# Performance work log

Measured on AMD Instinct MI355X. Metric: run time of the kernel, lower is better.

## Reference

```python
import jax, jax.numpy as jnp
import numpy as np

N_FEATURES = 64
HIDDEN = 512
BATCH = 128
SEQ = 1024


def _lstm_cell(x, h, c, w_ih, w_hh, b_ih, b_hh):
    # PyTorch gate order: input, forget, cell(g), output
    gates = x @ w_ih.T + b_ih + h @ w_hh.T + b_hh  # [B, 4H]
    i, f, g, o = jnp.split(gates, 4, axis=-1)
    c_new = jax.nn.sigmoid(f) * c + jax.nn.sigmoid(i) * jnp.tanh(g)
    h_new = jax.nn.sigmoid(o) * jnp.tanh(c_new)
    return h_new, c_new


def setup_inputs() -> dict:
    key = jax.random.key(0)
    ks = jax.random.split(key, 12)
    s_in = 1.0 / np.sqrt(HIDDEN)
    ts_batch = jax.random.normal(ks[0], (BATCH, SEQ, N_FEATURES), dtype=jnp.float32)
    u = lambda k, shape: jax.random.uniform(k, shape, jnp.float32, -s_in, s_in)
    return {
        "ts_batch": ts_batch,
        "w_ih_enc": u(ks[1], (4 * HIDDEN, N_FEATURES)),
        "w_hh_enc": u(ks[2], (4 * HIDDEN, HIDDEN)),
        "b_ih_enc": u(ks[3], (4 * HIDDEN,)),
        "b_hh_enc": u(ks[4], (4 * HIDDEN,)),
        "w_ih_dec": u(ks[5], (4 * HIDDEN, N_FEATURES)),
        "w_hh_dec": u(ks[6], (4 * HIDDEN, HIDDEN)),
        "b_ih_dec": u(ks[7], (4 * HIDDEN,)),
        "b_hh_dec": u(ks[8], (4 * HIDDEN,)),
        "w_out": u(ks[9], (N_FEATURES, HIDDEN)),
        "b_out": u(ks[10], (N_FEATURES,)),
    }


def reference(ts_batch, w_ih_enc, w_hh_enc, b_ih_enc, b_hh_enc,
              w_ih_dec, w_hh_dec, b_ih_dec, b_hh_dec, w_out, b_out):
    B, T, F = ts_batch.shape
    H = w_hh_enc.shape[1]
    h0 = jnp.zeros((B, H), ts_batch.dtype)
    c0 = jnp.zeros((B, H), ts_batch.dtype)

    # ---- encoder: run LSTM over time, keep final hidden state ----
    def enc_step(carry, x_t):
        h, c = carry
        h, c = _lstm_cell(x_t, h, c, w_ih_enc, w_hh_enc, b_ih_enc, b_hh_enc)
        return (h, c), None

    xs = jnp.transpose(ts_batch, (1, 0, 2))  # [T, B, F]
    (h_enc, _), _ = jax.lax.scan(enc_step, (h0, c0), xs)

    # ---- decoder (eval mode): reversed time, feed own output back ----
    def dec_step(carry, _):
        h, c = carry
        y = h @ w_out.T + b_out  # [B, F], emitted BEFORE the cell update
        h, c = _lstm_cell(y, h, c, w_ih_dec, w_hh_dec, b_ih_dec, b_hh_dec)
        return (h, c), y

    (_, _), ys = jax.lax.scan(dec_step, (h_enc, c0), None, length=T)
    # ys[k] corresponds to output time index T-1-k -> flip to chronological order
    output = jnp.transpose(ys[::-1], (1, 0, 2))  # [B, T, F]
    return output
```

## Files before the change

### kernel.cpp

```cpp
#include <hip/hip_runtime.h>
#include <math.h>

#define BB 128
#define TT 1024
#define FF 64
#define HH 512
#define G4 2048
#define NI 8
#define NJ 32
#define BT 16
#define NBLK 256
#define LDK 520
#define SENT 0xFFFFFFFFu

typedef float f32x4 __attribute__((ext_vector_type(4)));
typedef short s16x8 __attribute__((ext_vector_type(8)));
typedef unsigned short u16;
typedef unsigned int u32;
typedef unsigned long long u64;

__device__ u16 g_tsh[BB * TT * FF];
__device__ u16 g_tsl[BB * TT * FF];
__device__ float g_wihe[G4 * FF];
__device__ float g_whhe[G4 * HH];
__device__ float g_bihe[G4], g_bhhe[G4], g_bihd[G4], g_bhhd[G4];
__device__ float g_wihd[G4 * FF];
__device__ float g_whhd[G4 * HH];
__device__ float g_wout[FF * HH];
__device__ float g_bout[FF];
__device__ float g_weff[G4 * HH];
__device__ float g_beff[G4];
__device__ __align__(16) u64 g_hpak[2 * BB * HH];
__device__ __align__(16) float g_part[4 * NI * NJ * BT * FF];
__device__ int   g_isbf16;

__device__ __forceinline__ float bf2f(u16 u) {
  union { unsigned u; float f; } x; x.u = ((unsigned)u) << 16; return x.f;
}
__device__ __forceinline__ u16 f2bf(float f) {
  union { float f; unsigned u; } x; x.f = f;
  unsigned r = x.u + 0x7fffu + ((x.u >> 16) & 1u);
  return (u16)(r >> 16);
}
__device__ __forceinline__ float fsig(float x) {
  return __builtin_amdgcn_rcpf(1.f + __expf(-x));
}
__device__ __forceinline__ float ftanh(float x) {
  return 1.f - 2.f * __builtin_amdgcn_rcpf(__expf(2.f * x) + 1.f);
}

__global__ void sniff_kernel(const void* wout) {
  __shared__ int cnt[64];
  int t = threadIdx.x;
  const unsigned* d = (const unsigned*)wout;
  int c = 0;
  for (int k = t; k < 1024; k += 64) {
    unsigned b = (d[k] >> 8) & 0x7fu;
    c += (b >= 0x30u && b <= 0x3eu) ? 1 : 0;
  }
  cnt[t] = c;
  __syncthreads();
  if (t == 0) {
    int s = 0;
    for (int k = 0; k < 64; ++k) s += cnt[k];
    g_isbf16 = (s > 512) ? 1 : 0;
  }
}

__global__ void convert_kernel(const void* __restrict__ src, int which, int n) {
  int idx = blockIdx.x * 256 + threadIdx.x;
  if (idx >= n) return;
  float v;
  if (g_isbf16) v = bf2f(((const u16*)src)[idx]);
  else          v = ((const float*)src)[idx];
  if (which == 0) {
    u16 hi = f2bf(v);
    g_tsh[idx] = hi;
    g_tsl[idx] = f2bf(v - bf2f(hi));
    return;
  }
  float* dst;
  switch (which) {
    case 1: dst = g_wihe; break;
    case 2: dst = g_whhe; break;
    case 3: dst = g_bihe; break;
    case 4: dst = g_bhhe; break;
    case 5: dst = g_wihd; break;
    case 6: dst = g_whhd; break;
    case 7: dst = g_bihd; break;
    case 8: dst = g_bhhd; break;
    case 9: dst = g_wout; break;
    default: dst = g_bout; break;
  }
  dst[idx] = v;
}

__global__ void prep_kernel() {
  int idx = blockIdx.x * 256 + threadIdx.x;
  int r = idx >> 9, c = idx & 511;
  float acc = g_whhd[idx];
  const float* wr = &g_wihd[r * FF];
  for (int f = 0; f < FF; ++f) acc += wr[f] * g_wout[f * HH + c];
  g_weff[idx] = acc;
  if (idx < G4) {
    float b = g_bihd[idx] + g_bhhd[idx];
    for (int f = 0; f < FF; ++f) b += g_wihd[idx * FF + f] * g_bout[f];
    g_beff[idx] = b;
  }
}

__global__ void hinit_kernel() {
  int idx = blockIdx.x * 256 + threadIdx.x;
  g_hpak[idx] = (idx < (BB * HH / 2)) ? 0ull : 0xFFFFFFFFFFFFFFFFull;
}

#define MFMA __builtin_amdgcn_mfma_f32_16x16x32_bf16
#define A_LD(p)  __hip_atomic_load((p), __ATOMIC_RELAXED, __HIP_MEMORY_SCOPE_AGENT)
#define A_ST(p, v) __hip_atomic_store((p), (v), __ATOMIC_RELAXED, __HIP_MEMORY_SCOPE_AGENT)

#define BAR() do { asm volatile("s_waitcnt lgkmcnt(0)" ::: "memory"); \
                   __builtin_amdgcn_s_barrier(); } while (0)

#define LDR(R) do { \
    q[4*(R)+0] = A_LD(ph + (R)*256 +   0); \
    q[4*(R)+1] = A_LD(ph + (R)*256 +  64); \
    q[4*(R)+2] = A_LD(ph + (R)*256 + 128); \
    q[4*(R)+3] = A_LD(ph + (R)*256 + 192); } while (0)
#define BADR(R) ( ((u32)q[4*(R)+0]==SENT) | ((u32)(q[4*(R)+0]>>32)==SENT) | \
                  ((u32)q[4*(R)+1]==SENT) | ((u32)(q[4*(R)+1]>>32)==SENT) | \
                  ((u32)q[4*(R)+2]==SENT) | ((u32)(q[4*(R)+2]>>32)==SENT) | \
                  ((u32)q[4*(R)+3]==SENT) | ((u32)(q[4*(R)+3]>>32)==SENT) )

__global__ __launch_bounds__(256, 1) void lstm_persist(void* __restrict__ outv) {
  __shared__ u16 sHB[2][32 * LDK];
  __shared__ float sHn[16][17];
  __shared__ float sWoT[16][64];

  const int tid = threadIdx.x, bid = blockIdx.x;
  const int i = bid & 7, j = bid >> 3;
  const int wv = tid >> 6, lane = tid & 63;
  const int ln15 = lane & 15, lq = lane >> 4;
  const int gc = ln15 >> 2, uc = ln15 & 3;
  const int gr0 = gc * 512 + (j << 4) + (wv << 2) + uc;
  const int tb = gc;
  const int b_own = 4 * lq + tb;
  const int u_own = (wv << 2) + uc;
  const size_t colrow = (size_t)(i * BT + b_own) * (HH / 2) + (j << 3) + (u_own >> 1);
  const bool isbf = (g_isbf16 != 0);

  s16x8 wh[16], wl[16];
#pragma unroll
  for (int kt = 0; kt < 16; ++kt) {
    const float* p = &g_whhe[(size_t)gr0 * HH + kt * 32 + lq * 8];
#pragma unroll
    for (int q = 0; q < 8; ++q) {
      float w = p[q]; u16 hi = f2bf(w);
      wh[kt][q] = (short)hi; wl[kt][q] = (short)f2bf(w - bf2f(hi));
    }
  }
  s16x8 bxh0, bxh1, bxl0, bxl1;
  {
    const float* p0 = &g_wihe[(size_t)gr0 * FF + lq * 8];
#pragma unroll
    for (int q = 0; q < 8; ++q) {
      float w0 = p0[q], w1 = p0[32 + q];
      u16 h0 = f2bf(w0), h1 = f2bf(w1);
      bxh0[q] = (short)h0; bxl0[q] = (short)f2bf(w0 - bf2f(h0));
      bxh1[q] = (short)h1; bxl1[q] = (short)f2bf(w1 - bf2f(h1));
    }
  }
  for (int idx = tid; idx < 16 * 64; idx += 256) {
    int n = idx >> 6, f = idx & 63;
    sWoT[n][f] = g_wout[f * HH + (j << 4) + n];
  }
  float bias = g_bihe[gr0] + g_bhhe[gr0];

  const int e_jj = tid & 31;
  const int e_cell = (j << 3) + (tid >> 5);
  const int e_mm = e_cell >> 4, e_ff = (e_cell & 15) << 2;
  const float eb0 = g_bout[e_ff + 0], eb1 = g_bout[e_ff + 1];
  const float eb2 = g_bout[e_ff + 2], eb3 = g_bout[e_ff + 3];

  float c_st = 0.f;
  const int arow = ln15 * LDK;
  const int koff = lq * 8;

  for (int g = 0; g <= 2048; ++g) {
    const bool run = (g < 2048);
    float hn = 0.f;
    u64 e0 = 0, e1 = 0;
    const bool demit = (g >= 1025);

    if (!run && demit) {
      const int slot = (g - 2) & 3;
      const u64* psrc = (const u64*)&g_part[
          (size_t)((((slot * NI) + i) * NJ + e_jj) * BT + e_mm) * FF + e_ff];
      e0 = A_LD(psrc + 0); e1 = A_LD(psrc + 1);
    }

    if (run) {
      const bool enc = (g < 1024);
      s16x8 xh0 = {}, xl0 = {}, xh1 = {}, xl1 = {};
      if (enc) {
        const size_t xo = ((size_t)(i * BT + ln15) * TT + g) * FF + lq * 8;
        xh0 = *(const s16x8*)&g_tsh[xo];
        xh1 = *(const s16x8*)&g_tsh[xo + 32];
        xl0 = *(const s16x8*)&g_tsl[xo];
        xl1 = *(const s16x8*)&g_tsl[xo + 32];
      }

      u64 q[16];
      {
        const u64* ph = g_hpak
            + (size_t)((g & 3) * BB + i * BT + (wv << 2)) * (HH / 2) + lane;
        LDR(0); LDR(1); LDR(2); LDR(3);
        bool b0 = BADR(0), b1 = BADR(1), b2 = BADR(2), b3 = BADR(3);
        while (b0 | b1 | b2 | b3) {
          __builtin_amdgcn_s_sleep(1);
          if (b0) { LDR(0); b0 = BADR(0); }
          if (b1) { LDR(1); b1 = BADR(1); }
          if (b2) { LDR(2); b2 = BADR(2); }
          if (b3) { LDR(3); b3 = BADR(3); }
        }
      }
      {
        u16* sHw = &sHB[g & 1][0];
#pragma unroll
        for (int r = 0; r < 4; ++r) {
          const int row = (wv << 2) + r;
#pragma unroll
          for (int j2 = 0; j2 < 4; ++j2) {
            u64 v = q[4 * r + j2];
            u32 w0 = (u32)v, w1 = (u32)(v >> 32);
            u32 hi = __builtin_amdgcn_perm(w1, w0, 0x05040100u);
            u32 lo = __builtin_amdgcn_perm(w1, w0, 0x07060302u);
            const int u0 = 128 * j2 + 2 * lane;
            *(u32*)&sHw[row * LDK + u0] = hi;
            *(u32*)&sHw[(16 + row) * LDK + u0] = lo;
          }
        }
      }
      BAR();

      f32x4 a0a = {bias, bias, bias, bias};
      f32x4 a0b = {0.f,0.f,0.f,0.f}, a1a = {0.f,0.f,0.f,0.f}, a1b = {0.f,0.f,0.f,0.f};
      f32x4 a2a = {0.f,0.f,0.f,0.f}, a2b = {0.f,0.f,0.f,0.f};
      const u16* sHb = &sHB[g & 1][0];
#pragma unroll
      for (int kt = 0; kt < 16; kt += 2) {
        {
          s16x8 ah = *(const s16x8*)&sHb[arow + kt * 32 + koff];
          s16x8 al = *(const s16x8*)&sHb[16 * LDK + arow + kt * 32 + koff];
          a0a = MFMA(ah, wh[kt], a0a, 0, 0, 0);
          a1a = MFMA(al, wh[kt], a1a, 0, 0, 0);
          a2a = MFMA(ah, wl[kt], a2a, 0, 0, 0);
        }
        {
          s16x8 ah = *(const s16x8*)&sHb[arow + (kt + 1) * 32 + koff];
          s16x8 al = *(const s16x8*)&sHb[16 * LDK + arow + (kt + 1) * 32 + koff];
          a0b = MFMA(ah, wh[kt + 1], a0b, 0, 0, 0);
          a1b = MFMA(al, wh[kt + 1], a1b, 0, 0, 0);
          a2b = MFMA(ah, wl[kt + 1], a2b, 0, 0, 0);
        }
      }
      if (enc) {
        a0a = MFMA(xh0, bxh0, a0a, 0, 0, 0);
        a0b = MFMA(xh1, bxh1, a0b, 0, 0, 0);
        a1a = MFMA(xl0, bxh0, a1a, 0, 0, 0);
        a1b = MFMA(xl1, bxh1, a1b, 0, 0, 0);
        a2a = MFMA(xh0, bxl0, a2a, 0, 0, 0);
        a2b = MFMA(xh1, bxl1, a2b, 0, 0, 0);
      }
      f32x4 vs = (a0a + a0b) + (a1a + a1b) + (a2a + a2b);

      float A0 = vs.x, A1 = vs.y, A2 = vs.z, A3 = vs.w;
      float t0 = __shfl_xor(A2, 8), t1 = __shfl_xor(A3, 8);
      float t2 = __shfl_xor(A0, 8), t3 = __shfl_xor(A1, 8);
      const bool hi2 = (tb & 2) != 0;
      float B0 = hi2 ? t0 : A0, B1 = hi2 ? t1 : A1;
      float B2 = hi2 ? A2 : t2, B3 = hi2 ? A3 : t3;
      float u0 = __shfl_xor(B1, 4), u1 = __shfl_xor(B0, 4);
      float u2 = __shfl_xor(B3, 4), u3 = __shfl_xor(B2, 4);
      const bool hi1 = (tb & 1) != 0;
      float gi = hi1 ? u0 : B0, gf = hi1 ? B1 : u1;
      float gg = hi1 ? u2 : B2, go = hi1 ? B3 : u3;

      float si = fsig(gi), sf = fsig(gf), tg = ftanh(gg), so_ = fsig(go);
      c_st = sf * c_st + si * tg;
      hn = so_ * ftanh(c_st);
      {
        u16 h0p = f2bf(hn), l0p = f2bf(hn - bf2f(h0p));
        u32 pak = (u32)h0p | ((u32)l0p << 16);
        u32 oth = __shfl_down(pak, 1);
        asm volatile("s_waitcnt vmcnt(0)" ::: "memory");
        if ((ln15 & 1) == 0) {
          A_ST(&g_hpak[(size_t)(((g + 1) & 3)) * (BB * HH / 2) + colrow],
               (u64)pak | ((u64)oth << 32));
          A_ST(&g_hpak[(size_t)(((g + 3) & 3)) * (BB * HH / 2) + colrow],
               0xFFFFFFFFFFFFFFFFull);
        }
      }
      if (demit) {
        const int slot = (g - 2) & 3;
        const u64* psrc = (const u64*)&g_part[
            (size_t)((((slot * NI) + i) * NJ + e_jj) * BT + e_mm) * FF + e_ff];
        e0 = A_LD(psrc + 0); e1 = A_LD(psrc + 1);
      }
    }

    if (g >= 1023 && g < 2047) {
      sHn[b_own][u_own] = hn;
      BAR();
      const int fg = tid & 15, mm = tid >> 4;
      float p0 = 0.f, p1 = 0.f, p2 = 0.f, p3 = 0.f;
#pragma unroll
      for (int n = 0; n < 16; ++n) {
        float hv = sHn[mm][n];
        const f32x4 w = *(const f32x4*)&sWoT[n][fg << 2];
        p0 += hv * w.x; p1 += hv * w.y; p2 += hv * w.z; p3 += hv * w.w;
      }
      union { float f[4]; u64 d[2]; } pu;
      pu.f[0] = p0; pu.f[1] = p1; pu.f[2] = p2; pu.f[3] = p3;
      u64* pp = (u64*)&g_part[(size_t)((((g & 3) * NI + i) * NJ + j) * BT + mm) * FF + (fg << 2)];
      A_ST(pp + 0, pu.d[0]); A_ST(pp + 1, pu.d[1]);
    }
    if (demit) {
      const int k = g - 1025;
      union { u64 d[2]; float f[4]; } uu; uu.d[0] = e0; uu.d[1] = e1;
      float s0 = uu.f[0], s1 = uu.f[1], s2 = uu.f[2], s3 = uu.f[3];
#pragma unroll
      for (int m = 16; m >= 1; m >>= 1) {
        s0 += __shfl_xor(s0, m); s1 += __shfl_xor(s1, m);
        s2 += __shfl_xor(s2, m); s3 += __shfl_xor(s3, m);
      }
      if (e_jj == 0) {
        float o0 = s0 + eb0, o1 = s1 + eb1, o2 = s2 + eb2, o3 = s3 + eb3;
        size_t oidx = ((size_t)(i * BT + e_mm) * TT + (1023 - k)) * FF + e_ff;
        if (isbf) {
          union { u16 h[4]; u64 d; } ov;
          ov.h[0] = f2bf(o0); ov.h[1] = f2bf(o1); ov.h[2] = f2bf(o2); ov.h[3] = f2bf(o3);
          *(u64*)((u16*)outv + oidx) = ov.d;
        } else {
          f32x4 ov = {o0, o1, o2, o3};
          *(f32x4*)((float*)outv + oidx) = ov;
        }
      }
    }

    if (g == 1023) {
#pragma unroll
      for (int kt = 0; kt < 16; ++kt) {
        const float* p = &g_weff[(size_t)gr0 * HH + kt * 32 + lq * 8];
#pragma unroll
        for (int q2 = 0; q2 < 8; ++q2) {
          float w = p[q2]; u16 hi = f2bf(w);
          wh[kt][q2] = (short)hi; wl[kt][q2] = (short)f2bf(w - bf2f(hi));
        }
      }
      bias = g_beff[gr0];
      c_st = 0.f;
    }
  }
}

extern "C" void kernel_launch(void* const* d_in, const int* in_sizes, int n_in,
                              void* d_out, int out_size, void* d_ws, size_t ws_size,
                              hipStream_t stream) {
  sniff_kernel<<<1, 64, 0, stream>>>(d_in[9]);

  const int sizes[11] = { BB * TT * FF, G4 * FF, G4 * HH, G4, G4,
                          G4 * FF, G4 * HH, G4, G4, FF * HH, FF };
  for (int k = 0; k < 11; ++k)
    convert_kernel<<<(sizes[k] + 255) / 256, 256, 0, stream>>>(d_in[k], k, sizes[k]);

  prep_kernel<<<(G4 * HH) / 256, 256, 0, stream>>>();
  hinit_kernel<<<(2 * BB * HH) / 256, 256, 0, stream>>>();

  lstm_persist<<<NBLK, 256, 0, stream>>>(d_out);
}
```

Baseline: 6.235 ms.

## Halve persistent grid to 128 blocks of 512 threads, each owning 32 hidden units

The persistent LSTM kernel now runs 128 blocks of 8 waves instead of 256 blocks of 4 waves, so each block handles 32 hidden units per batch tile instead of 16. Each wave loads and spins on two rows of the shared hidden-state buffer instead of four. The output-projection partials are split into two half-blocks, which keeps the 32-way reduction layout unchanged. The aim is to halve the number of blocks polling global hidden-state flags and to cut redundant h reloads, at the cost of more register and LDS pressure per CU and half as many CUs in use.

```diff
diff --git a/kernel.cpp b/kernel.cpp
--- a/kernel.cpp
+++ b/kernel.cpp
@@ -8,8 +8,10 @@
 #define G4 2048
 #define NI 8
 #define NJ 32
+#define JB 16
 #define BT 16
-#define NBLK 256
+#define NBLK 128
+#define NTHR 512
 #define LDK 520
 #define SENT 0xFFFFFFFFu
 
@@ -32,7 +34,7 @@
 __device__ float g_beff[G4];
 __device__ __align__(16) u64 g_hpak[2 * BB * HH];
 __device__ __align__(16) float g_part[4 * NI * NJ * BT * FF];
-__device__ int   g_isbf16;
+__device__ int g_isbf16;
 
 __device__ __forceinline__ float bf2f(u16 u) {
   union { unsigned u; float f; } x; x.u = ((unsigned)u) << 16; return x.f;
@@ -131,21 +133,21 @@
                   ((u32)q[4*(R)+2]==SENT) | ((u32)(q[4*(R)+2]>>32)==SENT) | \
                   ((u32)q[4*(R)+3]==SENT) | ((u32)(q[4*(R)+3]>>32)==SENT) )
 
-__global__ __launch_bounds__(256, 1) void lstm_persist(void* __restrict__ outv) {
+__global__ __launch_bounds__(NTHR, 1) void lstm_persist(void* __restrict__ outv) {
   __shared__ u16 sHB[2][32 * LDK];
-  __shared__ float sHn[16][17];
-  __shared__ float sWoT[16][64];
+  __shared__ float sHn[16][33];
+  __shared__ float sWoT[32][64];
 
   const int tid = threadIdx.x, bid = blockIdx.x;
   const int i = bid & 7, j = bid >> 3;
   const int wv = tid >> 6, lane = tid & 63;
   const int ln15 = lane & 15, lq = lane >> 4;
   const int gc = ln15 >> 2, uc = ln15 & 3;
-  const int gr0 = gc * 512 + (j << 4) + (wv << 2) + uc;
+  const int gr0 = gc * 512 + (j << 5) + (wv << 2) + uc;
   const int tb = gc;
   const int b_own = 4 * lq + tb;
   const int u_own = (wv << 2) + uc;
-  const size_t colrow = (size_t)(i * BT + b_own) * (HH / 2) + (j << 3) + (u_own >> 1);
+  const size_t colrow = (size_t)(i * BT + b_own) * (HH / 2) + (j << 4) + (u_own >> 1);
   const bool isbf = (g_isbf16 != 0);
 
   s16x8 wh[16], wl[16];
@@ -153,33 +155,36 @@
   for (int kt = 0; kt < 16; ++kt) {
     const float* p = &g_whhe[(size_t)gr0 * HH + kt * 32 + lq * 8];
 #pragma unroll
-    for (int q = 0; q < 8; ++q) {
-      float w = p[q]; u16 hi = f2bf(w);
-      wh[kt][q] = (short)hi; wl[kt][q] = (short)f2bf(w - bf2f(hi));
+    for (int q2 = 0; q2 < 8; ++q2) {
+      float w = p[q2]; u16 hi = f2bf(w);
+      wh[kt][q2] = (short)hi; wl[kt][q2] = (short)f2bf(w - bf2f(hi));
     }
   }
   s16x8 bxh0, bxh1, bxl0, bxl1;
   {
     const float* p0 = &g_wihe[(size_t)gr0 * FF + lq * 8];
 #pragma unroll
-    for (int q = 0; q < 8; ++q) {
-      float w0 = p0[q], w1 = p0[32 + q];
+    for (int q2 = 0; q2 < 8; ++q2) {
+      float w0 = p0[q2], w1 = p0[32 + q2];
       u16 h0 = f2bf(w0), h1 = f2bf(w1);
-      bxh0[q] = (short)h0; bxl0[q] = (short)f2bf(w0 - bf2f(h0));
-      bxh1[q] = (short)h1; bxl1[q] = (short)f2bf(w1 - bf2f(h1));
-    }
-  }
-  for (int idx = tid; idx < 16 * 64; idx += 256) {
+      bxh0[q2] = (short)h0; bxl0[q2] = (short)f2bf(w0 - bf2f(h0));
+      bxh1[q2] = (short)h1; bxl1[q2] = (short)f2bf(w1 - bf2f(h1));
+    }
+  }
+  for (int idx = tid; idx < 32 * 64; idx += NTHR) {
     int n = idx >> 6, f = idx & 63;
-    sWoT[n][f] = g_wout[f * HH + (j << 4) + n];
+    sWoT[n][f] = g_wout[f * HH + (j << 5) + n];
   }
   float bias = g_bihe[gr0] + g_bhhe[gr0];
 
   const int e_jj = tid & 31;
-  const int e_cell = (j << 3) + (tid >> 5);
+  const int e_cell = (j << 4) + (tid >> 5);
   const int e_mm = e_cell >> 4, e_ff = (e_cell & 15) << 2;
   const float eb0 = g_bout[e_ff + 0], eb1 = g_bout[e_ff + 1];
   const float eb2 = g_bout[e_ff + 2], eb3 = g_bout[e_ff + 3];
+
+  const int p_fg = tid & 15, p_half = (tid >> 4) & 1, p_mm = tid >> 5;
+  const int p_n0 = p_half << 4;
 
   float c_st = 0.f;
   const int arow = ln15 * LDK;
@@ -209,32 +214,30 @@
         xl1 = *(const s16x8*)&g_tsl[xo + 32];
       }
 
-      u64 q[16];
+      u64 q[8];
       {
         const u64* ph = g_hpak
-            + (size_t)((g & 3) * BB + i * BT + (wv << 2)) * (HH / 2) + lane;
-        LDR(0); LDR(1); LDR(2); LDR(3);
-        bool b0 = BADR(0), b1 = BADR(1), b2 = BADR(2), b3 = BADR(3);
-        while (b0 | b1 | b2 | b3) {
+            + (size_t)((g & 3) * BB + i * BT + (wv << 1)) * (HH / 2) + lane;
+        LDR(0); LDR(1);
+        bool b0 = BADR(0), b1 = BADR(1);
+        while (b0 | b1) {
           __builtin_amdgcn_s_sleep(1);
           if (b0) { LDR(0); b0 = BADR(0); }
           if (b1) { LDR(1); b1 = BADR(1); }
-          if (b2) { LDR(2); b2 = BADR(2); }
-          if (b3) { LDR(3); b3 = BADR(3); }
         }
       }
       {
         u16* sHw = &sHB[g & 1][0];
 #pragma unroll
-        for (int r = 0; r < 4; ++r) {
-          const int row = (wv << 2) + r;
-#pragma unroll
-          for (int j2 = 0; j2 < 4; ++j2) {
-            u64 v = q[4 * r + j2];
+        for (int r = 0; r < 2; ++r) {
+          const int row = (wv << 1) + r;
+#pragma unroll
+          for (int k = 0; k < 4; ++k) {
+            u64 v = q[4 * r + k];
             u32 w0 = (u32)v, w1 = (u32)(v >> 32);
             u32 hi = __builtin_amdgcn_perm(w1, w0, 0x05040100u);
             u32 lo = __builtin_amdgcn_perm(w1, w0, 0x07060302u);
-            const int u0 = 128 * j2 + 2 * lane;
+            const int u0 = 128 * k + 2 * lane;
             *(u32*)&sHw[row * LDK + u0] = hi;
             *(u32*)&sHw[(16 + row) * LDK + u0] = lo;
           }
@@ -311,17 +314,17 @@
     if (g >= 1023 && g < 2047) {
       sHn[b_own][u_own] = hn;
       BAR();
-      const int fg = tid & 15, mm = tid >> 4;
       float p0 = 0.f, p1 = 0.f, p2 = 0.f, p3 = 0.f;
 #pragma unroll
       for (int n = 0; n < 16; ++n) {
-        float hv = sHn[mm][n];
-        const f32x4 w = *(const f32x4*)&sWoT[n][fg << 2];
+        float hv = sHn[p_mm][p_n0 + n];
+        const f32x4 w = *(const f32x4*)&sWoT[p_n0 + n][p_fg << 2];
         p0 += hv * w.x; p1 += hv * w.y; p2 += hv * w.z; p3 += hv * w.w;
       }
       union { float f[4]; u64 d[2]; } pu;
       pu.f[0] = p0; pu.f[1] = p1; pu.f[2] = p2; pu.f[3] = p3;
-      u64* pp = (u64*)&g_part[(size_t)((((g & 3) * NI + i) * NJ + j) * BT + mm) * FF + (fg << 2)];
+      u64* pp = (u64*)&g_part[(size_t)((((g & 3) * NI + i) * NJ + ((j << 1) + p_half))
+                                       * BT + p_mm) * FF + (p_fg << 2)];
       A_ST(pp + 0, pu.d[0]); A_ST(pp + 1, pu.d[1]);
     }
     if (demit) {
@@ -376,5 +379,5 @@
   prep_kernel<<<(G4 * HH) / 256, 256, 0, stream>>>();
   hinit_kernel<<<(2 * BB * HH) / 256, 256, 0, stream>>>();
 
-  lstm_persist<<<NBLK, 256, 0, stream>>>(d_out);
-}
+  lstm_persist<<<NBLK, NTHR, 0, stream>>>(d_out);
+}
```

New measurement: 9.499 ms. 1.52x slower.
